# Kernel tuning notes

Hardware: AMD Instinct MI355X
Metric: run time of the kernel (lower is better)

Reference implementation:

```python
import jax, jax.numpy as jnp
import numpy as np
from jax import lax

# --- static config (Detectron defaults, C4-style RPN) ---
B, A_NUM, H, W = 8, 15, 100, 168
STRIDE = 8.0                 # 1.0 / spatial_scale
PRE_NMS = 2000               # RPN_PRE_NMS_TOP_N
POST_NMS = 1000              # RPN_POST_NMS_TOP_N
NMS_THRESH = 0.7
MIN_SIZE = 0.0
BBOX_XFORM_CLIP = float(np.log(1000.0 / 16.0))


def _make_anchors():
    sizes = np.array([32., 64., 128., 256., 512.])
    ratios = np.array([0.5, 1.0, 2.0])
    out = []
    for s in sizes:
        for r in ratios:
            w = s * np.sqrt(1.0 / r)
            h = s * np.sqrt(r)
            out.append([-(w - 1) / 2., -(h - 1) / 2., (w - 1) / 2., (h - 1) / 2.])
    return np.asarray(out, dtype=np.float32)  # [15, 4]


def setup_inputs() -> dict:
    key = jax.random.key(0)
    k1, k2 = jax.random.split(key)
    rpn_cls_prob = jax.random.uniform(k1, (B, A_NUM, H, W), jnp.float32)
    rpn_bbox_pred = jax.random.normal(k2, (B, 4 * A_NUM, H, W), jnp.float32) * 0.1
    im_info = jnp.tile(jnp.array([[H * STRIDE, W * STRIDE, 1.0]], jnp.float32), (B, 1))
    anchors = jnp.asarray(_make_anchors())
    return {"rpn_cls_prob": rpn_cls_prob, "rpn_bbox_pred": rpn_bbox_pred,
            "im_info": im_info, "anchors": anchors}


def _bbox_transform(anchors, deltas):
    # Detectron bbox_transform with weights (1,1,1,1)
    ws = anchors[:, 2] - anchors[:, 0] + 1.0
    hs = anchors[:, 3] - anchors[:, 1] + 1.0
    cx = anchors[:, 0] + 0.5 * ws
    cy = anchors[:, 1] + 0.5 * hs
    dx, dy = deltas[:, 0], deltas[:, 1]
    dw = jnp.minimum(deltas[:, 2], BBOX_XFORM_CLIP)
    dh = jnp.minimum(deltas[:, 3], BBOX_XFORM_CLIP)
    pcx = dx * ws + cx
    pcy = dy * hs + cy
    pw = jnp.exp(dw) * ws
    ph = jnp.exp(dh) * hs
    return jnp.stack([pcx - 0.5 * pw, pcy - 0.5 * ph,
                      pcx + 0.5 * pw - 1.0, pcy + 0.5 * ph - 1.0], axis=1)


def _nms_keep(boxes, valid, thresh):
    # Greedy NMS on score-sorted boxes, fixed-shape via lax.scan.
    P = boxes.shape[0]
    x1, y1, x2, y2 = boxes[:, 0], boxes[:, 1], boxes[:, 2], boxes[:, 3]
    areas = (x2 - x1 + 1.0) * (y2 - y1 + 1.0)
    iw = jnp.maximum(jnp.minimum(x2[:, None], x2[None, :]) - jnp.maximum(x1[:, None], x1[None, :]) + 1.0, 0.0)
    ih = jnp.maximum(jnp.minimum(y2[:, None], y2[None, :]) - jnp.maximum(y1[:, None], y1[None, :]) + 1.0, 0.0)
    inter = iw * ih
    iou = inter / (areas[:, None] + areas[None, :] - inter)  # [P, P]
    idxs = jnp.arange(P)

    def step(suppressed, inp):
        row, is_valid, i = inp
        keep_i = is_valid & (~suppressed[i])
        suppressed = suppressed | (keep_i & (row > thresh) & (idxs > i))
        return suppressed, keep_i

    _, keep = lax.scan(step, jnp.zeros((P,), bool), (iou, valid, idxs))
    return keep


def _one_image(scores, deltas, iminfo, all_anchors):
    # scores: [A,H,W], deltas: [4A,H,W] -> flat (h, w, a) ordering, matching
    # all_anchors built as (K, A) with K = h*W + w.
    scores_f = jnp.transpose(scores, (1, 2, 0)).reshape(-1)          # [K*A]
    deltas_f = jnp.transpose(deltas, (1, 2, 0)).reshape(-1, 4)       # [K*A, 4]
    top_s, top_i = lax.top_k(scores_f, PRE_NMS)
    props = _bbox_transform(all_anchors[top_i], deltas_f[top_i])
    # clip_tiled_boxes to image bounds
    wmax, hmax = iminfo[1] - 1.0, iminfo[0] - 1.0
    x1 = jnp.clip(props[:, 0], 0.0, wmax)
    y1 = jnp.clip(props[:, 1], 0.0, hmax)
    x2 = jnp.clip(props[:, 2], 0.0, wmax)
    y2 = jnp.clip(props[:, 3], 0.0, hmax)
    props = jnp.stack([x1, y1, x2, y2], axis=1)
    # _filter_boxes (mask instead of drop, for fixed shapes)
    ws = x2 - x1 + 1.0
    hs = y2 - y1 + 1.0
    ms = MIN_SIZE * iminfo[2]
    valid = (ws >= ms) & (hs >= ms) & ((x1 + ws / 2.0) < iminfo[1]) & ((y1 + hs / 2.0) < iminfo[0])
    keep = _nms_keep(props, valid, NMS_THRESH)
    # kept boxes first (stable sort preserves descending-score order), take POST_NMS
    order = jnp.argsort(jnp.where(keep, 0, 1).astype(jnp.int32))[:POST_NMS]
    kept = keep[order]
    boxes = jnp.where(kept[:, None], props[order], 0.0)
    probs = jnp.where(kept, top_s[order], 0.0)
    return boxes, probs


def reference(rpn_cls_prob, rpn_bbox_pred, im_info, anchors):
    shift_x = jnp.arange(W, dtype=jnp.float32) * STRIDE
    shift_y = jnp.arange(H, dtype=jnp.float32) * STRIDE
    sx, sy = jnp.meshgrid(shift_x, shift_y)                 # [H, W] each
    shifts = jnp.stack([sx.ravel(), sy.ravel(), sx.ravel(), sy.ravel()], axis=1)  # [K, 4]
    all_anchors = (anchors[None, :, :] + shifts[:, None, :]).reshape(-1, 4)       # [K*A, 4]
    boxes, probs = jax.vmap(_one_image, in_axes=(0, 0, 0, None))(
        rpn_cls_prob, rpn_bbox_pred, im_info, all_anchors)      # [B,P,4], [B,P]
    binds = jnp.broadcast_to(jnp.arange(B, dtype=jnp.float32)[:, None, None], (B, POST_NMS, 1))
    rois = jnp.concatenate([binds, boxes], axis=2).reshape(B * POST_NMS, 5)
    return rois, probs.reshape(-1)
```

## Files before the change

### kernel.cpp

```cpp
#include <hip/hip_runtime.h>
#include <hip/hip_bf16.h>
#include <math.h>

#define BN 8
#define AN 15
#define HH 100
#define WW 168
#define HW (HH*WW)
#define NPI (AN*HW)
#define NTOT (BN*NPI)
#define PRE 2000
#define POST 1000
#define CAP 4096
#define ROWW 32
#define NCHUNK 32
#define RSTRIDE 2048
#define EPB 4096
#define HBLK 62
#define GELEM 2048
#define GBLK 124

typedef unsigned int u32;
typedef unsigned long long u64;

#define OFF_H1     0
#define OFF_H2     507904
#define OFF_CSTAR  1015808
#define OFF_CCNT   1016832
#define OFF_THR    1017856
#define OFF_CAND   1018880
#define OFF_BOX    1281024
#define OFF_SCORE  1543168
#define OFF_VALID  1608704
#define OFF_MASK   1674240
#define OFF_DIAG   5868544

__device__ __forceinline__ u32 fmono(float s) {
  u32 u = __float_as_uint(s);
  return (u & 0x80000000u) ? ~u : (u | 0x80000000u);
}
__device__ __forceinline__ float funmono(u32 m) {
  u32 u = (m & 0x80000000u) ? (m ^ 0x80000000u) : ~m;
  return __uint_as_float(u);
}
__device__ __forceinline__ float areaf(float4 bx) {
  return __fmul_rn(__fadd_rn(__fsub_rn(bx.z, bx.x), 1.0f),
                   __fadd_rn(__fsub_rn(bx.w, bx.y), 1.0f));
}

#define BAR_LGKM() asm volatile("s_waitcnt lgkmcnt(0)\ns_barrier" ::: "memory")

__device__ __forceinline__ u32 wave_suffix_incl(u32 v, int lane) {
  for (int d = 1; d < 64; d <<= 1) {
    u32 n = (u32)__shfl_down((int)v, d, 64);
    if (lane + d < 64) v += n;
  }
  return v;
}

__device__ __forceinline__ u64 shfl_xor64(u64 v, int m) {
  return (u64)__shfl_xor((unsigned long long)v, m, 64);
}

__global__ __launch_bounds__(256) void hist1_kernel(const float* __restrict__ cls,
                                                    u32* __restrict__ h1) {
  __shared__ u32 lh[16 * 258];
  int b = blockIdx.y;
  int t = threadIdx.x;
  for (int q = t; q < 16 * 258; q += 256) lh[q] = 0u;
  __syncthreads();
  int start = blockIdx.x * EPB;
  const float* p = cls + (size_t)b * NPI;
  u32 copy = ((u32)t & 15u) * 258u;
  if (start + EPB <= NPI) {
    const float4* p4 = (const float4*)(p + start);
#pragma unroll
    for (int q = 0; q < 4; ++q) {
      float4 v = p4[q * 256 + t];
      atomicAdd(&lh[copy + (fmono(v.x) >> 24)], 1u);
      atomicAdd(&lh[copy + (fmono(v.y) >> 24)], 1u);
      atomicAdd(&lh[copy + (fmono(v.z) >> 24)], 1u);
      atomicAdd(&lh[copy + (fmono(v.w) >> 24)], 1u);
    }
  } else {
    int end = NPI;
    for (int i = start + t; i < end; i += 256) {
      u32 m = fmono(p[i]);
      atomicAdd(&lh[copy + (m >> 24)], 1u);
    }
  }
  __syncthreads();
  u32 s = 0;
#pragma unroll
  for (int cpy = 0; cpy < 16; ++cpy) s += lh[cpy * 258 + t];
  h1[((size_t)(b * HBLK) + blockIdx.x) * 256 + t] = s;
}

__global__ __launch_bounds__(256) void coarse_kernel(const u32* __restrict__ h1,
                                                     u32* __restrict__ cstar) {
  int b = blockIdx.x;
  int t = threadIdx.x;
  __shared__ u32 cnts[256];
  u32 s = 0;
  for (int blk = 0; blk < HBLK; ++blk) s += h1[((size_t)(b * HBLK) + blk) * 256 + t];
  cnts[t] = s;
  __syncthreads();
  if (t < 64) {
    int lane = t;
    u32 v0 = cnts[4 * lane + 0], v1 = cnts[4 * lane + 1];
    u32 v2 = cnts[4 * lane + 2], v3 = cnts[4 * lane + 3];
    u32 ls3 = v3, ls2 = v2 + ls3, ls1 = v1 + ls2, ls0 = v0 + ls1;
    u32 incl = wave_suffix_incl(ls0, lane);
    u32 tail = incl - ls0;
    u32 s0 = tail + ls0, s1 = tail + ls1, s2 = tail + ls2, s3 = tail + ls3;
    u32 e0 = 4 * (u32)lane;
    if (lane == 0 && s0 < (u32)PRE) { cstar[b * 32] = 0u; cstar[b * 32 + 1] = s1; }
    if (s0 >= (u32)PRE && s1 < (u32)PRE) { cstar[b * 32] = e0 + 0; cstar[b * 32 + 1] = s1; }
    if (s1 >= (u32)PRE && s2 < (u32)PRE) { cstar[b * 32] = e0 + 1; cstar[b * 32 + 1] = s2; }
    if (s2 >= (u32)PRE && s3 < (u32)PRE) { cstar[b * 32] = e0 + 2; cstar[b * 32 + 1] = s3; }
    if (s3 >= (u32)PRE && (e0 + 3 == 255u || tail < (u32)PRE)) {
      cstar[b * 32] = e0 + 3;
      cstar[b * 32 + 1] = (e0 + 3 == 255u) ? 0u : tail;
    }
  }
}

__global__ __launch_bounds__(256) void hist2_kernel(const float* __restrict__ cls,
                                                    const u32* __restrict__ cstar,
                                                    u32* __restrict__ h2) {
  __shared__ u32 lh[4 * 260];
  int b = blockIdx.y;
  int t = threadIdx.x;
  for (int q = t; q < 4 * 260; q += 256) lh[q] = 0u;
  __syncthreads();
  u32 cs = cstar[b * 32];
  int start = blockIdx.x * EPB;
  const float* p = cls + (size_t)b * NPI;
  u32 copy = ((u32)t & 3u) * 260u;
  if (start + EPB <= NPI) {
    const float4* p4 = (const float4*)(p + start);
#pragma unroll
    for (int q = 0; q < 4; ++q) {
      float4 v = p4[q * 256 + t];
      u32 m;
      m = fmono(v.x); if ((m >> 24) == cs) atomicAdd(&lh[copy + ((m >> 16) & 0xFFu)], 1u);
      m = fmono(v.y); if ((m >> 24) == cs) atomicAdd(&lh[copy + ((m >> 16) & 0xFFu)], 1u);
      m = fmono(v.z); if ((m >> 24) == cs) atomicAdd(&lh[copy + ((m >> 16) & 0xFFu)], 1u);
      m = fmono(v.w); if ((m >> 24) == cs) atomicAdd(&lh[copy + ((m >> 16) & 0xFFu)], 1u);
    }
  } else {
    int end = NPI;
    for (int i = start + t; i < end; i += 256) {
      u32 m = fmono(p[i]);
      if ((m >> 24) == cs) atomicAdd(&lh[copy + ((m >> 16) & 0xFFu)], 1u);
    }
  }
  __syncthreads();
  u32 s = 0;
#pragma unroll
  for (int cpy = 0; cpy < 4; ++cpy) s += lh[cpy * 260 + t];
  h2[((size_t)(b * HBLK) + blockIdx.x) * 256 + t] = s;
}

__global__ __launch_bounds__(256) void fine_kernel(const u32* __restrict__ h2,
                                                   const u32* __restrict__ cstar,
                                                   u32* __restrict__ thr,
                                                   u32* __restrict__ ccnt) {
  int b = blockIdx.x;
  int t = threadIdx.x;
  __shared__ u32 cnts[256];
  u32 s = 0;
  for (int blk = 0; blk < HBLK; ++blk) s += h2[((size_t)(b * HBLK) + blk) * 256 + t];
  cnts[t] = s;
  __syncthreads();
  if (t == 64) ccnt[b * 32] = 0u;
  if (t < 64) {
    int lane = t;
    u32 cs = cstar[b * 32], base = cstar[b * 32 + 1];
    u32 v0 = cnts[4 * lane + 0], v1 = cnts[4 * lane + 1];
    u32 v2 = cnts[4 * lane + 2], v3 = cnts[4 * lane + 3];
    u32 ls3 = v3, ls2 = v2 + ls3, ls1 = v1 + ls2, ls0 = v0 + ls1;
    u32 incl = wave_suffix_incl(ls0, lane);
    u32 tail = incl - ls0;
    u32 s0 = base + tail + ls0, s1 = base + tail + ls1;
    u32 s2 = base + tail + ls2, s3 = base + tail + ls3;
    u32 sn = base + tail;
    u32 e0 = 4 * (u32)lane;
    if (lane == 0 && s0 < (u32)PRE) thr[b * 32] = (cs << 8);
    if (s0 >= (u32)PRE && s1 < (u32)PRE) thr[b * 32] = (cs << 8) | (e0 + 0);
    if (s1 >= (u32)PRE && s2 < (u32)PRE) thr[b * 32] = (cs << 8) | (e0 + 1);
    if (s2 >= (u32)PRE && s3 < (u32)PRE) thr[b * 32] = (cs << 8) | (e0 + 2);
    if (s3 >= (u32)PRE && (e0 + 3 == 255u || sn < (u32)PRE)) thr[b * 32] = (cs << 8) | (e0 + 3);
  }
}

__global__ __launch_bounds__(256) void gather_kernel(
    const float* __restrict__ cls, const u32* __restrict__ thr,
    u32* __restrict__ ccnt, u64* __restrict__ cand) {
  int b = blockIdx.y;
  int t = threadIdx.x;
  int lane = t & 63, wid = t >> 6;
  int base_i = blockIdx.x * GELEM;
  const float* p = cls + (size_t)b * NPI;
  u32 T = thr[b * 32];
  __shared__ int wsum[4];
  __shared__ int wbase[4];
  __shared__ u32 baseSh;

  u32 mv[8];
  u32 flags = 0;
  bool vec = (base_i + GELEM <= NPI);
  if (vec) {
    const float4* p4 = (const float4*)(p + base_i);
    float4 a = p4[t], c = p4[256 + t];
#pragma unroll
    for (int k = 0; k < 4; ++k) {
      float vv = (k == 0) ? a.x : (k == 1) ? a.y : (k == 2) ? a.z : a.w;
      u32 m = fmono(vv);
      mv[k] = m;
      flags |= ((m >> 16) >= T) ? (1u << k) : 0u;
    }
#pragma unroll
    for (int k = 0; k < 4; ++k) {
      float vv = (k == 0) ? c.x : (k == 1) ? c.y : (k == 2) ? c.z : c.w;
      u32 m = fmono(vv);
      mv[4 + k] = m;
      flags |= ((m >> 16) >= T) ? (1u << (4 + k)) : 0u;
    }
  } else {
#pragma unroll
    for (int k = 0; k < 8; ++k) {
      int i = base_i + k * 256 + t;
      u32 m = 0;
      bool ok = false;
      if (i < NPI) { m = fmono(p[i]); ok = (m >> 16) >= T; }
      mv[k] = m;
      flags |= ok ? (1u << k) : 0u;
    }
  }
  int ct = (int)__popc(flags);
  int inc = ct;
  for (int d = 1; d < 64; d <<= 1) {
    int n = __shfl_up(inc, d, 64);
    if (lane >= d) inc += n;
  }
  int excl = inc - ct;
  if (lane == 63) wsum[wid] = inc;
  __syncthreads();
  if (t == 0) {
    int acc = 0;
#pragma unroll
    for (int w = 0; w < 4; ++w) { wbase[w] = acc; acc += wsum[w]; }
    baseSh = acc ? atomicAdd(&ccnt[b * 32], (u32)acc) : 0u;
  }
  __syncthreads();
  if (!flags) return;
  u32 pos0 = baseSh + (u32)wbase[wid] + (u32)excl;
#pragma unroll
  for (int k = 0; k < 8; ++k) {
    if ((flags >> k) & 1u) {
      u32 pos = pos0 + (u32)__popc(flags & ((1u << k) - 1u));
      if (pos < CAP) {
        int i = vec ? (base_i + (k < 4 ? 4 * t + k : 1024 + 4 * t + (k - 4)))
                    : (base_i + k * 256 + t);
        int a = i / HW;
        int hw = i - a * HW;
        u32 ti = (u32)(hw * AN + a);
        cand[(size_t)b * CAP + pos] = ((u64)mv[k] << 32) | (u32)(~ti);
      }
    }
  }
}

__device__ __forceinline__ void transform_one(
    u64 key, int q, int b, u32 cnt,
    float im_h, float im_w, float wmax, float hmax, float msz,
    const float* __restrict__ bbox, const float* __restrict__ anch,
    float4* __restrict__ boxes, float* __restrict__ scores, int* __restrict__ valid) {
  const float BCLIP = (float)4.135166556742356;
  u32 i = ~((u32)key);
  if (q >= (int)cnt || i >= (u32)NPI) {
    boxes[b * RSTRIDE + q] = make_float4(0.f, 0.f, 0.f, 0.f);
    scores[b * RSTRIDE + q] = 0.f;
    valid[b * RSTRIDE + q] = 0;
    return;
  }
  float sc = funmono((u32)(key >> 32));
  int a = (int)(i % AN);
  int pp = (int)(i / AN);
  int w = pp % WW;
  int h = pp / WW;
  float sx = (float)(w * 8), sy = (float)(h * 8);
  float ax1 = __fadd_rn(anch[a * 4 + 0], sx);
  float ay1 = __fadd_rn(anch[a * 4 + 1], sy);
  float ax2 = __fadd_rn(anch[a * 4 + 2], sx);
  float ay2 = __fadd_rn(anch[a * 4 + 3], sy);
  float wsA = __fadd_rn(__fsub_rn(ax2, ax1), 1.0f);
  float hsA = __fadd_rn(__fsub_rn(ay2, ay1), 1.0f);
  float cx = __fadd_rn(ax1, __fmul_rn(0.5f, wsA));
  float cy = __fadd_rn(ay1, __fmul_rn(0.5f, hsA));
  const float* dp = bbox + ((size_t)b * (4 * AN) + 4 * a) * HW + (size_t)h * WW + w;
// ... 28 lines not shown
    const u32* __restrict__ thr,
    const float* __restrict__ bbox, const float* __restrict__ iminfo,
    const float* __restrict__ anch,
    float4* __restrict__ boxes, float* __restrict__ scores, int* __restrict__ valid) {
  __shared__ u64 keys[CAP];
  __shared__ u64 keys2[2048];
  __shared__ u32 h24[256];
  __shared__ u32 aboveSh, cmpCnt, t24Sh, cnt2Sh;
  int b = blockIdx.x;
  int t = threadIdx.x;
  int lane = t & 63;
  u32 cnt = ccnt[b * 32];
  if (cnt > CAP) cnt = CAP;
  u32 thr16v = thr[b * 32];
  for (int q = t; q < CAP; q += 1024) keys[q] = (q < (int)cnt) ? cand[(size_t)b * CAP + q] : 0ULL;
  keys2[t] = 0ULL; keys2[t + 1024] = 0ULL;
  if (t < 256) h24[t] = 0u;
  if (t == 0) { aboveSh = 0u; cmpCnt = 0u; }
  __syncthreads();

  for (int q0 = 0; q0 < CAP; q0 += 1024) {
    int q = q0 + t;
    u64 key = keys[q];
    u32 hi = (u32)(key >> 32);
    bool isReal = (q < (int)cnt);
    bool above = isReal && ((hi >> 16) > thr16v);
    u64 bal = __ballot(above);
    if (lane == 0 && bal) atomicAdd(&aboveSh, (u32)__popcll(bal));
    if (isReal && !above) atomicAdd(&h24[(hi >> 8) & 0xFFu], 1u);
  }
  __syncthreads();
  if (t < 64) {
    u32 basev = aboveSh;
    u32 v0 = h24[4 * lane + 0], v1 = h24[4 * lane + 1];
    u32 v2 = h24[4 * lane + 2], v3 = h24[4 * lane + 3];
    u32 ls3 = v3, ls2 = v2 + ls3, ls1 = v1 + ls2, ls0 = v0 + ls1;
    u32 incl = wave_suffix_incl(ls0, lane);
    u32 tail = incl - ls0;
    u32 s0 = basev + tail + ls0, s1 = basev + tail + ls1;
    u32 s2 = basev + tail + ls2, s3 = basev + tail + ls3;
    u32 sn = basev + tail;
    u32 e0 = 4 * (u32)lane;
    if (lane == 0 && s0 < (u32)PRE) { t24Sh = 0u; cnt2Sh = s0; }
    if (s0 >= (u32)PRE && s1 < (u32)PRE) { t24Sh = e0 + 0; cnt2Sh = s0; }
    if (s1 >= (u32)PRE && s2 < (u32)PRE) { t24Sh = e0 + 1; cnt2Sh = s1; }
    if (s2 >= (u32)PRE && s3 < (u32)PRE) { t24Sh = e0 + 2; cnt2Sh = s2; }
    if (s3 >= (u32)PRE && (e0 + 3 == 255u || sn < (u32)PRE)) { t24Sh = e0 + 3; cnt2Sh = s3; }
  }
  __syncthreads();
  u32 cnt2 = cnt2Sh;
  bool fallback = (cnt2 > 2048u);

  float im_h = iminfo[b * 3 + 0], im_w = iminfo[b * 3 + 1], im_s = iminfo[b * 3 + 2];
  float wmax = __fsub_rn(im_w, 1.0f), hmax = __fsub_rn(im_h, 1.0f);
  float msz = __fmul_rn(0.0f, im_s);

  if (!fallback) {
    u32 t24 = (thr16v << 8) | t24Sh;
    for (int q0 = 0; q0 < CAP; q0 += 1024) {
      int q = q0 + t;
      u64 key = keys[q];
      u32 hi = (u32)(key >> 32);
      bool pass = (q < (int)cnt) && ((hi >> 8) >= t24);
      u64 bal = __ballot(pass);
      if (bal) {
        u32 wb = 0;
        if (lane == 0) wb = atomicAdd(&cmpCnt, (u32)__popcll(bal));
        wb = (u32)__shfl((int)wb, 0, 64);
        if (pass) {
          u32 rank = (u32)__popcll(bal & ((1ULL << lane) - 1ULL));
          keys2[wb + rank] = key;
        }
      }
    }
    __syncthreads();
    u64 e0 = keys2[2 * t], e1 = keys2[2 * t + 1];
    for (u32 k = 2; k <= 2048; k <<= 1) {
      u32 kb = k >> 1;
      for (u32 j = k >> 1; j >= 1; j >>= 1) {
        bool up = ((u32)t & kb) == 0;
        if (j >= 128) {
          keys2[2 * t] = e0; keys2[2 * t + 1] = e1;
          __syncthreads();
          int pt = t ^ (int)(j >> 1);
          u64 y0 = keys2[2 * pt], y1 = keys2[2 * pt + 1];
          bool low = ((u32)t & (j >> 1)) == 0;
          bool mx = (up == low);
          e0 = mx ? (e0 > y0 ? e0 : y0) : (e0 < y0 ? e0 : y0);
          e1 = mx ? (e1 > y1 ? e1 : y1) : (e1 < y1 ? e1 : y1);
          __syncthreads();
        } else if (j >= 2) {
          int m = (int)(j >> 1);
          u64 y0 = shfl_xor64(e0, m), y1 = shfl_xor64(e1, m);
          bool low = ((u32)t & (u32)m) == 0;
          bool mx = (up == low);
          e0 = mx ? (e0 > y0 ? e0 : y0) : (e0 < y0 ? e0 : y0);
          e1 = mx ? (e1 > y1 ? e1 : y1) : (e1 < y1 ? e1 : y1);
        } else {
          u64 mx64 = (e0 > e1) ? e0 : e1;
          u64 mn64 = (e0 > e1) ? e1 : e0;
          e0 = up ? mx64 : mn64;
          e1 = up ? mn64 : mx64;
        }
      }
    }
    if (2 * t < PRE) {
      transform_one(e0, 2 * t, b, cnt, im_h, im_w, wmax, hmax, msz,
                    bbox, anch, boxes, scores, valid);
      transform_one(e1, 2 * t + 1, b, cnt, im_h, im_w, wmax, hmax, msz,
                    bbox, anch, boxes, scores, valid);
    }
  } else {
    for (u32 k = 2; k <= CAP; k <<= 1) {
      for (u32 j = k >> 1; j > 0; j >>= 1) {
        for (int p = 0; p < CAP / 2 / 1024; ++p) {
          u32 idx = (u32)t + (u32)p * 1024u;
          u32 base2 = ((idx & ~(j - 1)) << 1) | (idx & (j - 1));
          u32 partner = base2 + j;
          bool up2 = ((base2 & k) == 0);
          u64 A = keys[base2], Bv = keys[partner];
          bool sw = up2 ? (A < Bv) : (A > Bv);
          if (sw) { keys[base2] = Bv; keys[partner] = A; }
        }
        __syncthreads();
      }
    }
    for (int q = t; q < PRE; q += 1024)
// ... 30 lines not shown
    if (j <= i) continue;
    float4 bj = jbox[jj];
    float iw = fmaxf(__fadd_rn(__fsub_rn(fminf(bi.z, bj.z), fmaxf(bi.x, bj.x)), 1.0f), 0.0f);
    float ih = fmaxf(__fadd_rn(__fsub_rn(fminf(bi.w, bj.w), fmaxf(bi.y, bj.y)), 1.0f), 0.0f);
    float inter = __fmul_rn(iw, ih);
    float denom = __fsub_rn(__fadd_rn(ai, jarea[jj]), inter);
    float iou = inter / denom;
    if (iou > 0.7f) word |= (1ULL << jj);
  }
  mask[((size_t)(b * RSTRIDE) + i) * ROWW + jb] = word;
  if (jb == ib) diag[(size_t)b * RSTRIDE + i] = word;
}

__global__ __launch_bounds__(512) void seq_nms_kernel(
    const u64* __restrict__ mask, const u64* __restrict__ diag,
    const int* __restrict__ valid,
    const float4* __restrict__ boxes, const float* __restrict__ scores,
    float* __restrict__ out) {
  int b = blockIdx.x;
  int tid = threadIdx.x;
  int wid = tid >> 6, lane = tid & 63, lw = lane & 31, hf = lane >> 5;
  __shared__ u64 partial[16];
  __shared__ u64 keepbLDS;
  __shared__ u64 vbufLDS[NCHUNK];
  __shared__ u64 kbits_s[NCHUNK];
  __shared__ int chunkoff[NCHUNK];
  __shared__ int keeplist[PRE];
  __shared__ int Ksh;
  __shared__ int stopSh;

  if (tid < 16) partial[tid] = 0ULL;
  if (tid < NCHUNK) kbits_s[tid] = 0ULL;
  if (tid == 0) stopSh = 0;
  if (wid == 0) {
    for (int c = 0; c < NCHUNK; ++c) {
      int q = c * 64 + lane;
      int v = (q < PRE) ? valid[b * RSTRIDE + q] : 0;
      u64 bl = __ballot(v != 0);
      if (lane == 0) vbufLDS[c] = bl;
    }
  }
  __syncthreads();

  const u64* base = mask + (size_t)b * RSTRIDE * ROWW;
  const u64* dg = diag + (size_t)b * RSTRIDE;

  u64 rem = 0ULL;
  u64 Dv = 0ULL;
  if (wid == 0) Dv = dg[lane];
  int rb0 = wid * 8 + hf;
  int tot = 0;
  u64 cur0 = base[(size_t)(rb0 + 0) * ROWW + lw];
  u64 cur1 = base[(size_t)(rb0 + 2) * ROWW + lw];
  u64 cur2 = base[(size_t)(rb0 + 4) * ROWW + lw];
  u64 cur3 = base[(size_t)(rb0 + 6) * ROWW + lw];
  for (int c = 0; c < NCHUNK; ++c) {
    u64 n0 = 0, n1 = 0, n2 = 0, n3 = 0, Dnext = 0ULL;
    if (c + 1 < NCHUNK) {
      int c0n = (c + 1) * 64;
      n0 = base[(size_t)(c0n + rb0 + 0) * ROWW + lw];
      n1 = base[(size_t)(c0n + rb0 + 2) * ROWW + lw];
      n2 = base[(size_t)(c0n + rb0 + 4) * ROWW + lw];
      n3 = base[(size_t)(c0n + rb0 + 6) * ROWW + lw];
      if (wid == 0) Dnext = dg[(size_t)(c + 1) * 64 + lane];
    }
    if (wid == 0) {
      u64 nz = __ballot(Dv != 0ULL);
      u64 cv = partial[0];
#pragma unroll
      for (int s = 1; s < 16; ++s) cv |= partial[s];
      u32 clo = (u32)__builtin_amdgcn_readfirstlane((int)(u32)cv);
      u32 chi = (u32)__builtin_amdgcn_readfirstlane((int)(u32)(cv >> 32));
      u64 cl = ((u64)chi << 32) | clo;
// ... 52 lines not shown
    if ((word >> lane) & 1ULL) {
      int rank = (int)__popcll(word & ((1ULL << lane) - 1ULL));
      keeplist[chunkoff[c] + rank] = c * 64 + lane;
    }
  }
  __syncthreads();
  int K = Ksh;

  float* rois = out;
  float* probs = out + (size_t)BN * POST * 5;
  for (int r = tid; r < POST; r += 512) {
    float x1 = 0.f, y1 = 0.f, x2 = 0.f, y2 = 0.f, pr = 0.f;
    if (r < K) {
      int i = keeplist[r];
      float4 bb = boxes[b * RSTRIDE + i];
      x1 = bb.x; y1 = bb.y; x2 = bb.z; y2 = bb.w;
      pr = scores[b * RSTRIDE + i];
    }
    size_t ro = (size_t)(b * POST + r) * 5;
    rois[ro + 0] = (float)b;
    rois[ro + 1] = x1; rois[ro + 2] = y1; rois[ro + 3] = x2; rois[ro + 4] = y2;
    probs[b * POST + r] = pr;
  }
}

extern "C" void kernel_launch(void* const* d_in, const int* in_sizes, int n_in,
                              void* d_out, int out_size, void* d_ws, size_t ws_size,
                              hipStream_t stream) {
  const float* cls    = (const float*)d_in[0];
  const float* bbox   = (const float*)d_in[1];
  const float* iminfo = (const float*)d_in[2];
  const float* anch   = (const float*)d_in[3];
  char* ws = (char*)d_ws;
  u32* h1    = (u32*)(ws + OFF_H1);
  u32* h2    = (u32*)(ws + OFF_H2);
  u32* cstar = (u32*)(ws + OFF_CSTAR);
  u32* ccnt  = (u32*)(ws + OFF_CCNT);
  u32* thr   = (u32*)(ws + OFF_THR);
  u64* cand  = (u64*)(ws + OFF_CAND);
  float4* boxes = (float4*)(ws + OFF_BOX);
  float* scores = (float*)(ws + OFF_SCORE);
  int* valid    = (int*)(ws + OFF_VALID);
  u64* mask     = (u64*)(ws + OFF_MASK);
  u64* diag     = (u64*)(ws + OFF_DIAG);
  float* out = (float*)d_out;

  hist1_kernel<<<dim3(HBLK, BN), 256, 0, stream>>>(cls, h1);
  coarse_kernel<<<BN, 256, 0, stream>>>(h1, cstar);
  hist2_kernel<<<dim3(HBLK, BN), 256, 0, stream>>>(cls, cstar, h2);
  fine_kernel<<<BN, 256, 0, stream>>>(h2, cstar, thr, ccnt);
  gather_kernel<<<dim3(GBLK, BN), 256, 0, stream>>>(cls, thr, ccnt, cand);
  sort_transform_kernel<<<BN, 1024, 0, stream>>>(cand, ccnt, thr, bbox, iminfo, anch,
                                                 boxes, scores, valid);
  nms_mask_kernel<<<dim3(528, BN), 64, 0, stream>>>(boxes, mask, diag);
  seq_nms_kernel<<<BN, 512, 0, stream>>>(mask, diag, valid, boxes, scores, out);
}
```

Measured before the change: 177.7 us.

## Fuse top-k threshold selection passes into one cooperative kernel with grid syncs

Replaces five kernels (two histogram passes, two scan kernels, gather) with one cooperative-launch kernel. Each block loads its score slice into registers once and reuses it for both histogram passes and the candidate gather, with grid.sync between phases and global atomics merging the per-block histograms. This removes four kernel launches and two extra reads of the score tensor, at the cost of grid-wide barriers, global atomic contention and reliance on all 496 blocks being co-resident. It also spreads the valid-bit ballot in the NMS kernel across all waves instead of one.

```diff
diff --git a/kernel.cpp b/kernel.cpp
--- a/kernel.cpp
+++ b/kernel.cpp
@@ -1,6 +1,9 @@
 #include <hip/hip_runtime.h>
 #include <hip/hip_bf16.h>
+#include <hip/hip_cooperative_groups.h>
 #include <math.h>
+
+namespace cg = cooperative_groups;
 
 #define BN 8
 #define AN 15
@@ -8,7 +11,6 @@
 #define WW 168
 #define HW (HH*WW)
 #define NPI (AN*HW)
-#define NTOT (BN*NPI)
 #define PRE 2000
 #define POST 1000
 #define CAP 4096
@@ -17,14 +19,12 @@
 #define RSTRIDE 2048
 #define EPB 4096
 #define HBLK 62
-#define GELEM 2048
-#define GBLK 124
 
 typedef unsigned int u32;
 typedef unsigned long long u64;
 
 #define OFF_H1     0
-#define OFF_H2     507904
+#define OFF_H2     8192
 #define OFF_CSTAR  1015808
 #define OFF_CCNT   1016832
 #define OFF_THR    1017856
@@ -62,181 +62,130 @@
   return (u64)__shfl_xor((unsigned long long)v, m, 64);
 }
 
-__global__ __launch_bounds__(256) void hist1_kernel(const float* __restrict__ cls,
-                                                    u32* __restrict__ h1) {
+__device__ __forceinline__ int sel_idx(bool vecp, int start, int t, int k) {
+  return vecp ? (start + 1024 * (k >> 2) + 4 * t + (k & 3))
+              : (start + k * 256 + t);
+}
+
+__global__ __launch_bounds__(256) void select_kernel(
+    const float* __restrict__ cls,
+    u32* __restrict__ h1g, u32* __restrict__ h2g,
+    u32* __restrict__ thr, u32* __restrict__ ccnt, u64* __restrict__ cand) {
+  cg::grid_group grid = cg::this_grid();
   __shared__ u32 lh[16 * 258];
+  __shared__ u32 csSh, cbaseSh, thrSh;
+  __shared__ int wsum[4], wbase[4];
+  __shared__ u32 gbaseSh;
   int b = blockIdx.y;
+  int blk = blockIdx.x;
   int t = threadIdx.x;
-  for (int q = t; q < 16 * 258; q += 256) lh[q] = 0u;
-  __syncthreads();
-  int start = blockIdx.x * EPB;
+  int lane = t & 63, wid = t >> 6;
+
+  int gtid = (b * HBLK + blk) * 256 + t;
+  if (gtid < 2048) h1g[gtid] = 0u;
+  else if (gtid < 4096) h2g[gtid - 2048] = 0u;
+  else if (gtid < 4352) ccnt[gtid - 4096] = 0u;
+
+  int start = blk * EPB;
   const float* p = cls + (size_t)b * NPI;
-  u32 copy = ((u32)t & 15u) * 258u;
-  if (start + EPB <= NPI) {
+  bool vecp = (start + EPB <= NPI);
+  u32 m[16];
+  if (vecp) {
     const float4* p4 = (const float4*)(p + start);
 #pragma unroll
     for (int q = 0; q < 4; ++q) {
       float4 v = p4[q * 256 + t];
-      atomicAdd(&lh[copy + (fmono(v.x) >> 24)], 1u);
-      atomicAdd(&lh[copy + (fmono(v.y) >> 24)], 1u);
-      atomicAdd(&lh[copy + (fmono(v.z) >> 24)], 1u);
-      atomicAdd(&lh[copy + (fmono(v.w) >> 24)], 1u);
+      m[4 * q + 0] = fmono(v.x); m[4 * q + 1] = fmono(v.y);
+      m[4 * q + 2] = fmono(v.z); m[4 * q + 3] = fmono(v.w);
     }
   } else {
-    int end = NPI;
-    for (int i = start + t; i < end; i += 256) {
-      u32 m = fmono(p[i]);
-      atomicAdd(&lh[copy + (m >> 24)], 1u);
-    }
-  }
-  __syncthreads();
-  u32 s = 0;
-#pragma unroll
-  for (int cpy = 0; cpy < 16; ++cpy) s += lh[cpy * 258 + t];
-  h1[((size_t)(b * HBLK) + blockIdx.x) * 256 + t] = s;
-}
-
-__global__ __launch_bounds__(256) void coarse_kernel(const u32* __restrict__ h1,
-                                                     u32* __restrict__ cstar) {
-  int b = blockIdx.x;
-  int t = threadIdx.x;
-  __shared__ u32 cnts[256];
-  u32 s = 0;
-  for (int blk = 0; blk < HBLK; ++blk) s += h1[((size_t)(b * HBLK) + blk) * 256 + t];
-  cnts[t] = s;
-  __syncthreads();
+#pragma unroll
+    for (int k = 0; k < 16; ++k) {
+      int i = start + k * 256 + t;
+      m[k] = (i < NPI) ? fmono(p[i]) : 0u;
+    }
+  }
+
+  for (int q = t; q < 16 * 258; q += 256) lh[q] = 0u;
+  __syncthreads();
+  u32 copy = ((u32)t & 15u) * 258u;
+#pragma unroll
+  for (int k = 0; k < 16; ++k) {
+    int i = sel_idx(vecp, start, t, k);
+    if (i < NPI) atomicAdd(&lh[copy + (m[k] >> 24)], 1u);
+  }
+  __syncthreads();
+  u32 csum = 0;
+#pragma unroll
+  for (int c = 0; c < 16; ++c) csum += lh[c * 258 + t];
+
+  grid.sync();
+  if (csum) atomicAdd(&h1g[b * 256 + t], csum);
+  grid.sync();
+
   if (t < 64) {
-    int lane = t;
-    u32 v0 = cnts[4 * lane + 0], v1 = cnts[4 * lane + 1];
-    u32 v2 = cnts[4 * lane + 2], v3 = cnts[4 * lane + 3];
+    u32 v0 = h1g[b * 256 + 4 * t + 0], v1 = h1g[b * 256 + 4 * t + 1];
+    u32 v2 = h1g[b * 256 + 4 * t + 2], v3 = h1g[b * 256 + 4 * t + 3];
     u32 ls3 = v3, ls2 = v2 + ls3, ls1 = v1 + ls2, ls0 = v0 + ls1;
-    u32 incl = wave_suffix_incl(ls0, lane);
+    u32 incl = wave_suffix_incl(ls0, t);
     u32 tail = incl - ls0;
     u32 s0 = tail + ls0, s1 = tail + ls1, s2 = tail + ls2, s3 = tail + ls3;
-    u32 e0 = 4 * (u32)lane;
-    if (lane == 0 && s0 < (u32)PRE) { cstar[b * 32] = 0u; cstar[b * 32 + 1] = s1; }
-    if (s0 >= (u32)PRE && s1 < (u32)PRE) { cstar[b * 32] = e0 + 0; cstar[b * 32 + 1] = s1; }
-    if (s1 >= (u32)PRE && s2 < (u32)PRE) { cstar[b * 32] = e0 + 1; cstar[b * 32 + 1] = s2; }
-    if (s2 >= (u32)PRE && s3 < (u32)PRE) { cstar[b * 32] = e0 + 2; cstar[b * 32 + 1] = s3; }
+    u32 e0 = 4 * (u32)t;
+    if (t == 0 && s0 < (u32)PRE) { csSh = 0u; cbaseSh = s1; }
+    if (s0 >= (u32)PRE && s1 < (u32)PRE) { csSh = e0 + 0; cbaseSh = s1; }
+    if (s1 >= (u32)PRE && s2 < (u32)PRE) { csSh = e0 + 1; cbaseSh = s2; }
+    if (s2 >= (u32)PRE && s3 < (u32)PRE) { csSh = e0 + 2; cbaseSh = s3; }
     if (s3 >= (u32)PRE && (e0 + 3 == 255u || tail < (u32)PRE)) {
-      cstar[b * 32] = e0 + 3;
-      cstar[b * 32 + 1] = (e0 + 3 == 255u) ? 0u : tail;
-    }
-  }
-}
-
-__global__ __launch_bounds__(256) void hist2_kernel(const float* __restrict__ cls,
-                                                    const u32* __restrict__ cstar,
-                                                    u32* __restrict__ h2) {
-  __shared__ u32 lh[4 * 260];
-  int b = blockIdx.y;
-  int t = threadIdx.x;
+      csSh = e0 + 3;
+      cbaseSh = (e0 + 3 == 255u) ? 0u : tail;
+    }
+  }
+  __syncthreads();
+  u32 cs = csSh;
+
   for (int q = t; q < 4 * 260; q += 256) lh[q] = 0u;
   __syncthreads();
-  u32 cs = cstar[b * 32];
-  int start = blockIdx.x * EPB;
-  const float* p = cls + (size_t)b * NPI;
-  u32 copy = ((u32)t & 3u) * 260u;
-  if (start + EPB <= NPI) {
-    const float4* p4 = (const float4*)(p + start);
-#pragma unroll
-    for (int q = 0; q < 4; ++q) {
-      float4 v = p4[q * 256 + t];
-      u32 m;
-      m = fmono(v.x); if ((m >> 24) == cs) atomicAdd(&lh[copy + ((m >> 16) & 0xFFu)], 1u);
-      m = fmono(v.y); if ((m >> 24) == cs) atomicAdd(&lh[copy + ((m >> 16) & 0xFFu)], 1u);
-      m = fmono(v.z); if ((m >> 24) == cs) atomicAdd(&lh[copy + ((m >> 16) & 0xFFu)], 1u);
-      m = fmono(v.w); if ((m >> 24) == cs) atomicAdd(&lh[copy + ((m >> 16) & 0xFFu)], 1u);
-    }
-  } else {
-    int end = NPI;
-    for (int i = start + t; i < end; i += 256) {
-      u32 m = fmono(p[i]);
-      if ((m >> 24) == cs) atomicAdd(&lh[copy + ((m >> 16) & 0xFFu)], 1u);
-    }
-  }
-  __syncthreads();
-  u32 s = 0;
-#pragma unroll
-  for (int cpy = 0; cpy < 4; ++cpy) s += lh[cpy * 260 + t];
-  h2[((size_t)(b * HBLK) + blockIdx.x) * 256 + t] = s;
-}
-
-__global__ __launch_bounds__(256) void fine_kernel(const u32* __restrict__ h2,
-                                                   const u32* __restrict__ cstar,
-                                                   u32* __restrict__ thr,
-                                                   u32* __restrict__ ccnt) {
-  int b = blockIdx.x;
-  int t = threadIdx.x;
-  __shared__ u32 cnts[256];
-  u32 s = 0;
-  for (int blk = 0; blk < HBLK; ++blk) s += h2[((size_t)(b * HBLK) + blk) * 256 + t];
-  cnts[t] = s;
-  __syncthreads();
-  if (t == 64) ccnt[b * 32] = 0u;
+  u32 copy2 = ((u32)t & 3u) * 260u;
+#pragma unroll
+  for (int k = 0; k < 16; ++k) {
+    int i = sel_idx(vecp, start, t, k);
+    if (i < NPI && (m[k] >> 24) == cs)
+      atomicAdd(&lh[copy2 + ((m[k] >> 16) & 0xFFu)], 1u);
+  }
+  __syncthreads();
+  u32 fsum = 0;
+#pragma unroll
+  for (int c = 0; c < 4; ++c) fsum += lh[c * 260 + t];
+  if (fsum) atomicAdd(&h2g[b * 256 + t], fsum);
+  grid.sync();
+
   if (t < 64) {
-    int lane = t;
-    u32 cs = cstar[b * 32], base = cstar[b * 32 + 1];
-    u32 v0 = cnts[4 * lane + 0], v1 = cnts[4 * lane + 1];
-    u32 v2 = cnts[4 * lane + 2], v3 = cnts[4 * lane + 3];
+    u32 base = cbaseSh;
+    u32 v0 = h2g[b * 256 + 4 * t + 0], v1 = h2g[b * 256 + 4 * t + 1];
+    u32 v2 = h2g[b * 256 + 4 * t + 2], v3 = h2g[b * 256 + 4 * t + 3];
     u32 ls3 = v3, ls2 = v2 + ls3, ls1 = v1 + ls2, ls0 = v0 + ls1;
-    u32 incl = wave_suffix_incl(ls0, lane);
+    u32 incl = wave_suffix_incl(ls0, t);
     u32 tail = incl - ls0;
     u32 s0 = base + tail + ls0, s1 = base + tail + ls1;
     u32 s2 = base + tail + ls2, s3 = base + tail + ls3;
     u32 sn = base + tail;
-    u32 e0 = 4 * (u32)lane;
-    if (lane == 0 && s0 < (u32)PRE) thr[b * 32] = (cs << 8);
-    if (s0 >= (u32)PRE && s1 < (u32)PRE) thr[b * 32] = (cs << 8) | (e0 + 0);
-    if (s1 >= (u32)PRE && s2 < (u32)PRE) thr[b * 32] = (cs << 8) | (e0 + 1);
-    if (s2 >= (u32)PRE && s3 < (u32)PRE) thr[b * 32] = (cs << 8) | (e0 + 2);
-    if (s3 >= (u32)PRE && (e0 + 3 == 255u || sn < (u32)PRE)) thr[b * 32] = (cs << 8) | (e0 + 3);
-  }
-}
-
-__global__ __launch_bounds__(256) void gather_kernel(
-    const float* __restrict__ cls, const u32* __restrict__ thr,
-    u32* __restrict__ ccnt, u64* __restrict__ cand) {
-  int b = blockIdx.y;
-  int t = threadIdx.x;
-  int lane = t & 63, wid = t >> 6;
-  int base_i = blockIdx.x * GELEM;
-  const float* p = cls + (size_t)b * NPI;
-  u32 T = thr[b * 32];
-  __shared__ int wsum[4];
-  __shared__ int wbase[4];
-  __shared__ u32 baseSh;
-
-  u32 mv[8];
+    u32 e0 = 4 * (u32)t;
+    if (t == 0 && s0 < (u32)PRE) thrSh = (cs << 8);
+    if (s0 >= (u32)PRE && s1 < (u32)PRE) thrSh = (cs << 8) | (e0 + 0);
+    if (s1 >= (u32)PRE && s2 < (u32)PRE) thrSh = (cs << 8) | (e0 + 1);
+    if (s2 >= (u32)PRE && s3 < (u32)PRE) thrSh = (cs << 8) | (e0 + 2);
+    if (s3 >= (u32)PRE && (e0 + 3 == 255u || sn < (u32)PRE)) thrSh = (cs << 8) | (e0 + 3);
+  }
+  __syncthreads();
+  u32 T = thrSh;
+  if (blk == 0 && t == 0) thr[b * 32] = T;
+
   u32 flags = 0;
-  bool vec = (base_i + GELEM <= NPI);
-  if (vec) {
-    const float4* p4 = (const float4*)(p + base_i);
-    float4 a = p4[t], c = p4[256 + t];
-#pragma unroll
-    for (int k = 0; k < 4; ++k) {
-      float vv = (k == 0) ? a.x : (k == 1) ? a.y : (k == 2) ? a.z : a.w;
-      u32 m = fmono(vv);
-      mv[k] = m;
-      flags |= ((m >> 16) >= T) ? (1u << k) : 0u;
-    }
-#pragma unroll
-    for (int k = 0; k < 4; ++k) {
-      float vv = (k == 0) ? c.x : (k == 1) ? c.y : (k == 2) ? c.z : c.w;
-      u32 m = fmono(vv);
-      mv[4 + k] = m;
-      flags |= ((m >> 16) >= T) ? (1u << (4 + k)) : 0u;
-    }
-  } else {
-#pragma unroll
-    for (int k = 0; k < 8; ++k) {
-      int i = base_i + k * 256 + t;
-      u32 m = 0;
-      bool ok = false;
-      if (i < NPI) { m = fmono(p[i]); ok = (m >> 16) >= T; }
-      mv[k] = m;
-      flags |= ok ? (1u << k) : 0u;
-    }
+#pragma unroll
+  for (int k = 0; k < 16; ++k) {
+    int i = sel_idx(vecp, start, t, k);
+    bool ok = (i < NPI) && ((m[k] >> 16) >= T);
+    flags |= ok ? (1u << k) : 0u;
   }
   int ct = (int)__popc(flags);
   int inc = ct;
@@ -251,22 +200,21 @@
     int acc = 0;
 #pragma unroll
     for (int w = 0; w < 4; ++w) { wbase[w] = acc; acc += wsum[w]; }
-    baseSh = acc ? atomicAdd(&ccnt[b * 32], (u32)acc) : 0u;
+    gbaseSh = acc ? atomicAdd(&ccnt[b * 32], (u32)acc) : 0u;
   }
   __syncthreads();
   if (!flags) return;
-  u32 pos0 = baseSh + (u32)wbase[wid] + (u32)excl;
-#pragma unroll
-  for (int k = 0; k < 8; ++k) {
+  u32 pos0 = gbaseSh + (u32)wbase[wid] + (u32)excl;
+#pragma unroll
+  for (int k = 0; k < 16; ++k) {
     if ((flags >> k) & 1u) {
       u32 pos = pos0 + (u32)__popc(flags & ((1u << k) - 1u));
       if (pos < CAP) {
-        int i = vec ? (base_i + (k < 4 ? 4 * t + k : 1024 + 4 * t + (k - 4)))
-                    : (base_i + k * 256 + t);
+        int i = sel_idx(vecp, start, t, k);
         int a = i / HW;
         int hw = i - a * HW;
         u32 ti = (u32)(hw * AN + a);
-        cand[(size_t)b * CAP + pos] = ((u64)mv[k] << 32) | (u32)(~ti);
+        cand[(size_t)b * CAP + pos] = ((u64)m[k] << 32) | (u32)(~ti);
       }
     }
   }
@@ -361,16 +309,16 @@
   __syncthreads();
   if (t < 64) {
     u32 basev = aboveSh;
-    u32 v0 = h24[4 * lane + 0], v1 = h24[4 * lane + 1];
-    u32 v2 = h24[4 * lane + 2], v3 = h24[4 * lane + 3];
+    u32 v0 = h24[4 * t + 0], v1 = h24[4 * t + 1];
+    u32 v2 = h24[4 * t + 2], v3 = h24[4 * t + 3];
     u32 ls3 = v3, ls2 = v2 + ls3, ls1 = v1 + ls2, ls0 = v0 + ls1;
-    u32 incl = wave_suffix_incl(ls0, lane);
+    u32 incl = wave_suffix_incl(ls0, t);
     u32 tail = incl - ls0;
     u32 s0 = basev + tail + ls0, s1 = basev + tail + ls1;
     u32 s2 = basev + tail + ls2, s3 = basev + tail + ls3;
     u32 sn = basev + tail;
-    u32 e0 = 4 * (u32)lane;
-    if (lane == 0 && s0 < (u32)PRE) { t24Sh = 0u; cnt2Sh = s0; }
+    u32 e0 = 4 * (u32)t;
+    if (t == 0 && s0 < (u32)PRE) { t24Sh = 0u; cnt2Sh = s0; }
     if (s0 >= (u32)PRE && s1 < (u32)PRE) { t24Sh = e0 + 0; cnt2Sh = s0; }
     if (s1 >= (u32)PRE && s2 < (u32)PRE) { t24Sh = e0 + 1; cnt2Sh = s1; }
     if (s2 >= (u32)PRE && s3 < (u32)PRE) { t24Sh = e0 + 2; cnt2Sh = s2; }
@@ -419,9 +367,9 @@
           e1 = mx ? (e1 > y1 ? e1 : y1) : (e1 < y1 ? e1 : y1);
           __syncthreads();
         } else if (j >= 2) {
-          int m = (int)(j >> 1);
-          u64 y0 = shfl_xor64(e0, m), y1 = shfl_xor64(e1, m);
-          bool low = ((u32)t & (u32)m) == 0;
+          int mm = (int)(j >> 1);
+          u64 y0 = shfl_xor64(e0, mm), y1 = shfl_xor64(e1, mm);
+          bool low = ((u32)t & (u32)mm) == 0;
           bool mx = (up == low);
           e0 = mx ? (e0 > y0 ? e0 : y0) : (e0 < y0 ? e0 : y0);
           e1 = mx ? (e1 > y1 ? e1 : y1) : (e1 < y1 ? e1 : y1);
@@ -518,13 +466,11 @@
   if (tid < 16) partial[tid] = 0ULL;
   if (tid < NCHUNK) kbits_s[tid] = 0ULL;
   if (tid == 0) stopSh = 0;
-  if (wid == 0) {
-    for (int c = 0; c < NCHUNK; ++c) {
-      int q = c * 64 + lane;
-      int v = (q < PRE) ? valid[b * RSTRIDE + q] : 0;
-      u64 bl = __ballot(v != 0);
-      if (lane == 0) vbufLDS[c] = bl;
-    }
+  for (int c = wid * 4; c < wid * 4 + 4; ++c) {
+    int q = c * 64 + lane;
+    int v = (q < PRE) ? valid[b * RSTRIDE + q] : 0;
+    u64 bl = __ballot(v != 0);
+    if (lane == 0) vbufLDS[c] = bl;
   }
   __syncthreads();
 
@@ -643,9 +589,8 @@
   const float* iminfo = (const float*)d_in[2];
   const float* anch   = (const float*)d_in[3];
   char* ws = (char*)d_ws;
-  u32* h1    = (u32*)(ws + OFF_H1);
-  u32* h2    = (u32*)(ws + OFF_H2);
-  u32* cstar = (u32*)(ws + OFF_CSTAR);
+  u32* h1g   = (u32*)(ws + OFF_H1);
+  u32* h2g   = (u32*)(ws + OFF_H2);
   u32* ccnt  = (u32*)(ws + OFF_CCNT);
   u32* thr   = (u32*)(ws + OFF_THR);
   u64* cand  = (u64*)(ws + OFF_CAND);
@@ -656,11 +601,13 @@
   u64* diag     = (u64*)(ws + OFF_DIAG);
   float* out = (float*)d_out;
 
-  hist1_kernel<<<dim3(HBLK, BN), 256, 0, stream>>>(cls, h1);
-  coarse_kernel<<<BN, 256, 0, stream>>>(h1, cstar);
-  hist2_kernel<<<dim3(HBLK, BN), 256, 0, stream>>>(cls, cstar, h2);
-  fine_kernel<<<BN, 256, 0, stream>>>(h2, cstar, thr, ccnt);
-  gather_kernel<<<dim3(GBLK, BN), 256, 0, stream>>>(cls, thr, ccnt, cand);
+  const float* cls_ = cls;
+  u32 *h1g_ = h1g, *h2g_ = h2g, *thr_ = thr, *ccnt_ = ccnt;
+  u64* cand_ = cand;
+  void* args[] = {(void*)&cls_, (void*)&h1g_, (void*)&h2g_,
+                  (void*)&thr_, (void*)&ccnt_, (void*)&cand_};
+  hipLaunchCooperativeKernel((void*)select_kernel, dim3(HBLK, BN), dim3(256),
+                             args, 0, stream);
   sort_transform_kernel<<<BN, 1024, 0, stream>>>(cand, ccnt, thr, bbox, iminfo, anch,
                                                  boxes, scores, valid);
   nms_mask_kernel<<<dim3(528, BN), 64, 0, stream>>>(boxes, mask, diag);
```

Result: slower. 320.5 us (+80.4%).

## Fuse coarse and fine threshold scans into histogram and gather kernels

Applied to the files above, without the earlier changes.

Removes the single-block coarse and fine scan kernels by having every hist2 block and every gather block redundantly reduce the previous histogram and compute the radix threshold in shared memory. Block 0 still writes cstar, thr and resets ccnt for later stages. This cuts two kernel launches and their serialization gaps, at the cost of each block re-reading the full per-image histogram array from L2. The valid-bitmask build in the NMS kernel is also spread across all waves instead of one.

```diff
diff --git a/kernel.cpp b/kernel.cpp
--- a/kernel.cpp
+++ b/kernel.cpp
@@ -8,7 +8,6 @@
 #define WW 168
 #define HW (HH*WW)
 #define NPI (AN*HW)
-#define NTOT (BN*NPI)
 #define PRE 2000
 #define POST 1000
 #define CAP 4096
@@ -83,8 +82,7 @@
       atomicAdd(&lh[copy + (fmono(v.w) >> 24)], 1u);
     }
   } else {
-    int end = NPI;
-    for (int i = start + t; i < end; i += 256) {
+    for (int i = start + t; i < NPI; i += 256) {
       u32 m = fmono(p[i]);
       atomicAdd(&lh[copy + (m >> 24)], 1u);
     }
@@ -96,44 +94,45 @@
   h1[((size_t)(b * HBLK) + blockIdx.x) * 256 + t] = s;
 }
 
-__global__ __launch_bounds__(256) void coarse_kernel(const u32* __restrict__ h1,
-                                                     u32* __restrict__ cstar) {
-  int b = blockIdx.x;
+__global__ __launch_bounds__(256) void hist2_kernel(const float* __restrict__ cls,
+                                                    const u32* __restrict__ h1,
+                                                    u32* __restrict__ cstar,
+                                                    u32* __restrict__ ccnt,
+                                                    u32* __restrict__ h2) {
+  __shared__ u32 cnts[256];
+  __shared__ u32 csSh, cbaseSh;
+  __shared__ u32 lh[4 * 260];
+  int b = blockIdx.y;
   int t = threadIdx.x;
-  __shared__ u32 cnts[256];
   u32 s = 0;
   for (int blk = 0; blk < HBLK; ++blk) s += h1[((size_t)(b * HBLK) + blk) * 256 + t];
   cnts[t] = s;
   __syncthreads();
   if (t < 64) {
-    int lane = t;
-    u32 v0 = cnts[4 * lane + 0], v1 = cnts[4 * lane + 1];
-    u32 v2 = cnts[4 * lane + 2], v3 = cnts[4 * lane + 3];
+    u32 v0 = cnts[4 * t + 0], v1 = cnts[4 * t + 1];
+    u32 v2 = cnts[4 * t + 2], v3 = cnts[4 * t + 3];
     u32 ls3 = v3, ls2 = v2 + ls3, ls1 = v1 + ls2, ls0 = v0 + ls1;
-    u32 incl = wave_suffix_incl(ls0, lane);
+    u32 incl = wave_suffix_incl(ls0, t);
     u32 tail = incl - ls0;
     u32 s0 = tail + ls0, s1 = tail + ls1, s2 = tail + ls2, s3 = tail + ls3;
-    u32 e0 = 4 * (u32)lane;
-    if (lane == 0 && s0 < (u32)PRE) { cstar[b * 32] = 0u; cstar[b * 32 + 1] = s1; }
-    if (s0 >= (u32)PRE && s1 < (u32)PRE) { cstar[b * 32] = e0 + 0; cstar[b * 32 + 1] = s1; }
-    if (s1 >= (u32)PRE && s2 < (u32)PRE) { cstar[b * 32] = e0 + 1; cstar[b * 32 + 1] = s2; }
-    if (s2 >= (u32)PRE && s3 < (u32)PRE) { cstar[b * 32] = e0 + 2; cstar[b * 32 + 1] = s3; }
+    u32 e0 = 4 * (u32)t;
+    if (t == 0 && s0 < (u32)PRE) { csSh = 0u; cbaseSh = s1; }
+    if (s0 >= (u32)PRE && s1 < (u32)PRE) { csSh = e0 + 0; cbaseSh = s1; }
+    if (s1 >= (u32)PRE && s2 < (u32)PRE) { csSh = e0 + 1; cbaseSh = s2; }
+    if (s2 >= (u32)PRE && s3 < (u32)PRE) { csSh = e0 + 2; cbaseSh = s3; }
     if (s3 >= (u32)PRE && (e0 + 3 == 255u || tail < (u32)PRE)) {
-      cstar[b * 32] = e0 + 3;
-      cstar[b * 32 + 1] = (e0 + 3 == 255u) ? 0u : tail;
-    }
-  }
-}
-
-__global__ __launch_bounds__(256) void hist2_kernel(const float* __restrict__ cls,
-                                                    const u32* __restrict__ cstar,
-                                                    u32* __restrict__ h2) {
-  __shared__ u32 lh[4 * 260];
-  int b = blockIdx.y;
-  int t = threadIdx.x;
+      csSh = e0 + 3;
+      cbaseSh = (e0 + 3 == 255u) ? 0u : tail;
+    }
+  }
+  __syncthreads();
+  u32 cs = csSh;
+  if (blockIdx.x == 0 && t == 64) {
+    cstar[b * 32] = cs; cstar[b * 32 + 1] = cbaseSh;
+    ccnt[b * 32] = 0u;
+  }
   for (int q = t; q < 4 * 260; q += 256) lh[q] = 0u;
   __syncthreads();
-  u32 cs = cstar[b * 32];
   int start = blockIdx.x * EPB;
   const float* p = cls + (size_t)b * NPI;
   u32 copy = ((u32)t & 3u) * 260u;
@@ -149,64 +148,56 @@
       m = fmono(v.w); if ((m >> 24) == cs) atomicAdd(&lh[copy + ((m >> 16) & 0xFFu)], 1u);
     }
   } else {
-    int end = NPI;
-    for (int i = start + t; i < end; i += 256) {
+    for (int i = start + t; i < NPI; i += 256) {
       u32 m = fmono(p[i]);
       if ((m >> 24) == cs) atomicAdd(&lh[copy + ((m >> 16) & 0xFFu)], 1u);
     }
   }
   __syncthreads();
-  u32 s = 0;
-#pragma unroll
-  for (int cpy = 0; cpy < 4; ++cpy) s += lh[cpy * 260 + t];
-  h2[((size_t)(b * HBLK) + blockIdx.x) * 256 + t] = s;
-}
-
-__global__ __launch_bounds__(256) void fine_kernel(const u32* __restrict__ h2,
-                                                   const u32* __restrict__ cstar,
-                                                   u32* __restrict__ thr,
-                                                   u32* __restrict__ ccnt) {
-  int b = blockIdx.x;
+  u32 fs = 0;
+#pragma unroll
+  for (int cpy = 0; cpy < 4; ++cpy) fs += lh[cpy * 260 + t];
+  h2[((size_t)(b * HBLK) + blockIdx.x) * 256 + t] = fs;
+}
+
+__global__ __launch_bounds__(256) void gather_kernel(
+    const float* __restrict__ cls, const u32* __restrict__ h2,
+    const u32* __restrict__ cstar,
+    u32* __restrict__ thr, u32* __restrict__ ccnt, u64* __restrict__ cand) {
+  __shared__ u32 cnts[256];
+  __shared__ u32 thrSh;
+  __shared__ int wsum[4], wbase[4];
+  __shared__ u32 baseSh;
+  int b = blockIdx.y;
   int t = threadIdx.x;
-  __shared__ u32 cnts[256];
+  int lane = t & 63, wid = t >> 6;
   u32 s = 0;
   for (int blk = 0; blk < HBLK; ++blk) s += h2[((size_t)(b * HBLK) + blk) * 256 + t];
   cnts[t] = s;
   __syncthreads();
-  if (t == 64) ccnt[b * 32] = 0u;
   if (t < 64) {
-    int lane = t;
     u32 cs = cstar[b * 32], base = cstar[b * 32 + 1];
-    u32 v0 = cnts[4 * lane + 0], v1 = cnts[4 * lane + 1];
-    u32 v2 = cnts[4 * lane + 2], v3 = cnts[4 * lane + 3];
+    u32 v0 = cnts[4 * t + 0], v1 = cnts[4 * t + 1];
+    u32 v2 = cnts[4 * t + 2], v3 = cnts[4 * t + 3];
     u32 ls3 = v3, ls2 = v2 + ls3, ls1 = v1 + ls2, ls0 = v0 + ls1;
-    u32 incl = wave_suffix_incl(ls0, lane);
+    u32 incl = wave_suffix_incl(ls0, t);
     u32 tail = incl - ls0;
     u32 s0 = base + tail + ls0, s1 = base + tail + ls1;
     u32 s2 = base + tail + ls2, s3 = base + tail + ls3;
     u32 sn = base + tail;
-    u32 e0 = 4 * (u32)lane;
-    if (lane == 0 && s0 < (u32)PRE) thr[b * 32] = (cs << 8);
-    if (s0 >= (u32)PRE && s1 < (u32)PRE) thr[b * 32] = (cs << 8) | (e0 + 0);
-    if (s1 >= (u32)PRE && s2 < (u32)PRE) thr[b * 32] = (cs << 8) | (e0 + 1);
-    if (s2 >= (u32)PRE && s3 < (u32)PRE) thr[b * 32] = (cs << 8) | (e0 + 2);
-    if (s3 >= (u32)PRE && (e0 + 3 == 255u || sn < (u32)PRE)) thr[b * 32] = (cs << 8) | (e0 + 3);
-  }
-}
-
-__global__ __launch_bounds__(256) void gather_kernel(
-    const float* __restrict__ cls, const u32* __restrict__ thr,
-    u32* __restrict__ ccnt, u64* __restrict__ cand) {
-  int b = blockIdx.y;
-  int t = threadIdx.x;
-  int lane = t & 63, wid = t >> 6;
+    u32 e0 = 4 * (u32)t;
+    if (t == 0 && s0 < (u32)PRE) thrSh = (cs << 8);
+    if (s0 >= (u32)PRE && s1 < (u32)PRE) thrSh = (cs << 8) | (e0 + 0);
+    if (s1 >= (u32)PRE && s2 < (u32)PRE) thrSh = (cs << 8) | (e0 + 1);
+    if (s2 >= (u32)PRE && s3 < (u32)PRE) thrSh = (cs << 8) | (e0 + 2);
+    if (s3 >= (u32)PRE && (e0 + 3 == 255u || sn < (u32)PRE)) thrSh = (cs << 8) | (e0 + 3);
+  }
+  __syncthreads();
+  u32 T = thrSh;
+  if (blockIdx.x == 0 && t == 65) thr[b * 32] = T;
+
   int base_i = blockIdx.x * GELEM;
   const float* p = cls + (size_t)b * NPI;
-  u32 T = thr[b * 32];
-  __shared__ int wsum[4];
-  __shared__ int wbase[4];
-  __shared__ u32 baseSh;
-
   u32 mv[8];
   u32 flags = 0;
   bool vec = (base_i + GELEM <= NPI);
@@ -361,16 +352,16 @@
   __syncthreads();
   if (t < 64) {
     u32 basev = aboveSh;
-    u32 v0 = h24[4 * lane + 0], v1 = h24[4 * lane + 1];
-    u32 v2 = h24[4 * lane + 2], v3 = h24[4 * lane + 3];
+    u32 v0 = h24[4 * t + 0], v1 = h24[4 * t + 1];
+    u32 v2 = h24[4 * t + 2], v3 = h24[4 * t + 3];
     u32 ls3 = v3, ls2 = v2 + ls3, ls1 = v1 + ls2, ls0 = v0 + ls1;
-    u32 incl = wave_suffix_incl(ls0, lane);
+    u32 incl = wave_suffix_incl(ls0, t);
     u32 tail = incl - ls0;
     u32 s0 = basev + tail + ls0, s1 = basev + tail + ls1;
     u32 s2 = basev + tail + ls2, s3 = basev + tail + ls3;
     u32 sn = basev + tail;
-    u32 e0 = 4 * (u32)lane;
-    if (lane == 0 && s0 < (u32)PRE) { t24Sh = 0u; cnt2Sh = s0; }
+    u32 e0 = 4 * (u32)t;
+    if (t == 0 && s0 < (u32)PRE) { t24Sh = 0u; cnt2Sh = s0; }
     if (s0 >= (u32)PRE && s1 < (u32)PRE) { t24Sh = e0 + 0; cnt2Sh = s0; }
     if (s1 >= (u32)PRE && s2 < (u32)PRE) { t24Sh = e0 + 1; cnt2Sh = s1; }
     if (s2 >= (u32)PRE && s3 < (u32)PRE) { t24Sh = e0 + 2; cnt2Sh = s2; }
@@ -419,9 +410,9 @@
           e1 = mx ? (e1 > y1 ? e1 : y1) : (e1 < y1 ? e1 : y1);
           __syncthreads();
         } else if (j >= 2) {
-          int m = (int)(j >> 1);
-          u64 y0 = shfl_xor64(e0, m), y1 = shfl_xor64(e1, m);
-          bool low = ((u32)t & (u32)m) == 0;
+          int mm = (int)(j >> 1);
+          u64 y0 = shfl_xor64(e0, mm), y1 = shfl_xor64(e1, mm);
+          bool low = ((u32)t & (u32)mm) == 0;
           bool mx = (up == low);
           e0 = mx ? (e0 > y0 ? e0 : y0) : (e0 < y0 ? e0 : y0);
           e1 = mx ? (e1 > y1 ? e1 : y1) : (e1 < y1 ? e1 : y1);
@@ -518,13 +509,11 @@
   if (tid < 16) partial[tid] = 0ULL;
   if (tid < NCHUNK) kbits_s[tid] = 0ULL;
   if (tid == 0) stopSh = 0;
-  if (wid == 0) {
-    for (int c = 0; c < NCHUNK; ++c) {
-      int q = c * 64 + lane;
-      int v = (q < PRE) ? valid[b * RSTRIDE + q] : 0;
-      u64 bl = __ballot(v != 0);
-      if (lane == 0) vbufLDS[c] = bl;
-    }
+  for (int c = wid * 4; c < wid * 4 + 4; ++c) {
+    int q = c * 64 + lane;
+    int v = (q < PRE) ? valid[b * RSTRIDE + q] : 0;
+    u64 bl = __ballot(v != 0);
+    if (lane == 0) vbufLDS[c] = bl;
   }
   __syncthreads();
 
@@ -657,10 +646,8 @@
   float* out = (float*)d_out;
 
   hist1_kernel<<<dim3(HBLK, BN), 256, 0, stream>>>(cls, h1);
-  coarse_kernel<<<BN, 256, 0, stream>>>(h1, cstar);
-  hist2_kernel<<<dim3(HBLK, BN), 256, 0, stream>>>(cls, cstar, h2);
-  fine_kernel<<<BN, 256, 0, stream>>>(h2, cstar, thr, ccnt);
-  gather_kernel<<<dim3(GBLK, BN), 256, 0, stream>>>(cls, thr, ccnt, cand);
+  hist2_kernel<<<dim3(HBLK, BN), 256, 0, stream>>>(cls, h1, cstar, ccnt, h2);
+  gather_kernel<<<dim3(GBLK, BN), 256, 0, stream>>>(cls, h2, cstar, thr, ccnt, cand);
   sort_transform_kernel<<<BN, 1024, 0, stream>>>(cand, ccnt, thr, bbox, iminfo, anch,
                                                  boxes, scores, valid);
   nms_mask_kernel<<<dim3(528, BN), 64, 0, stream>>>(boxes, mask, diag);
```

Measured after the change: 169.7 us. 1.05x faster.
